# Optimization experiments

Hardware: AMD Instinct MI355X
Metric: run time of the kernel (lower is better)

## Reference

```python
import jax, jax.numpy as jnp
import numpy as np

B, L, D = 64, 4096, 256

def setup_inputs() -> dict:
    key = jax.random.key(0)
    k1, k2 = jax.random.split(key)
    inp = jax.random.normal(k1, (B, L, D), dtype=jnp.float32)
    # lengths in [1, L] so no empty-sequence mean (matches original assumption)
    length = jax.random.randint(k2, (B,), 1, L + 1, dtype=jnp.int64)
    return {"input": inp, "length": length}

def reference(input, length):
    # One fused masked mean over the ragged sequence dim.
    # mask: [B, L] True for valid positions
    mask = (jnp.arange(input.shape[1])[None, :] < length[:, None])
    m = mask.astype(input.dtype)[:, :, None]            # [B, L, 1]
    summed = jnp.sum(input * m, axis=1)                  # [B, D]
    return summed / length.astype(input.dtype)[:, None] # [B, D]
```

## Files before the change

kernel.cpp:

```cpp
#include <hip/hip_runtime.h>

#define BB 64
#define LL 4096
#define DD 256
#define D4 (DD / 4)
#define WAVES 4
#define RWAVES 8

template <int PP>
__global__ __launch_bounds__(256) void avg_partial_kernel(
    const float* __restrict__ in,
    const int* __restrict__ len,
    float* __restrict__ ws)
{
    constexpr int RPC = LL / PP;
    const int w    = threadIdx.x >> 6;
    const int lane = threadIdx.x & 63;
    const int c    = blockIdx.x * WAVES + w;
    const int b    = c / PP;
    const int p    = c % PP;

    const int lb   = len[b];
    const int row0 = p * RPC;
    if (row0 >= lb) return;

    int n = lb - row0;
    if (n > RPC) n = RPC;

    const float4* __restrict__ base =
        (const float4*)(in + (size_t)b * LL * DD) + (size_t)row0 * D4 + lane;

    float4 acc = make_float4(0.f, 0.f, 0.f, 0.f);
    #pragma unroll 8
    for (int r = 0; r < n; ++r) {
        float4 v = base[(size_t)r * D4];
        acc.x += v.x; acc.y += v.y; acc.z += v.z; acc.w += v.w;
    }

    float4* __restrict__ wsb = (float4*)ws + ((size_t)b * PP + p) * D4;
    wsb[lane] = acc;
}

template <int PP>
__global__ __launch_bounds__(512) void avg_reduce_kernel(
    const float* __restrict__ ws,
    const int* __restrict__ len,
    float* __restrict__ out)
{
    constexpr int RPC = LL / PP;
    const int b    = blockIdx.x;
    const int w    = threadIdx.x >> 6;
    const int lane = threadIdx.x & 63;

    int lb = len[b];
    if (lb < 1) lb = 1;
    const int nchunks = (lb + RPC - 1) / RPC;

    float4 acc = make_float4(0.f, 0.f, 0.f, 0.f);
    const float4* __restrict__ wsb = (const float4*)ws + (size_t)b * PP * D4;

    #pragma unroll 4
    for (int p = w; p < nchunks; p += RWAVES) {
        float4 v = wsb[(size_t)p * D4 + lane];
        acc.x += v.x; acc.y += v.y; acc.z += v.z; acc.w += v.w;
    }

    __shared__ float4 sh[RWAVES - 1][64];
    if (w > 0) sh[w - 1][lane] = acc;
    __syncthreads();

    if (w == 0) {
        #pragma unroll
        for (int i = 0; i < RWAVES - 1; ++i) {
            float4 v = sh[i][lane];
            acc.x += v.x; acc.y += v.y; acc.z += v.z; acc.w += v.w;
        }
        const float inv = 1.0f / (float)lb;
        float4 o = make_float4(acc.x * inv, acc.y * inv, acc.z * inv, acc.w * inv);
        ((float4*)out)[(size_t)b * D4 + lane] = o;
    }
}

__global__ void avg_zero_out_kernel(float* __restrict__ out) {
    int i = blockIdx.x * blockDim.x + threadIdx.x;
    if (i < BB * DD) out[i] = 0.f;
}

__global__ __launch_bounds__(64) void avg_atomic_kernel(
    const float* __restrict__ in,
    const int* __restrict__ len,
    float* __restrict__ out)
{
    const int b    = blockIdx.x >> 6;
    const int p    = blockIdx.x & 63;
    const int lane = threadIdx.x;

    int lb = len[b];
    if (lb < 1) lb = 1;
    const int row0 = p * 64;
    int rend = row0 + 64;
    if (rend > lb) rend = (lb > row0) ? lb : row0;
    if (rend <= row0) return;

    float4 acc = make_float4(0.f, 0.f, 0.f, 0.f);
    const float4* __restrict__ base = (const float4*)(in + (size_t)b * LL * DD);
    for (int r = row0; r < rend; ++r) {
        float4 v = base[(size_t)r * D4 + lane];
        acc.x += v.x; acc.y += v.y; acc.z += v.z; acc.w += v.w;
    }
    const float inv = 1.0f / (float)lb;
    float* o = out + (size_t)b * DD + lane * 4;
    atomicAdd(o + 0, acc.x * inv);
    atomicAdd(o + 1, acc.y * inv);
    atomicAdd(o + 2, acc.z * inv);
    atomicAdd(o + 3, acc.w * inv);
}

extern "C" void kernel_launch(void* const* d_in, const int* in_sizes, int n_in,
                              void* d_out, int out_size, void* d_ws, size_t ws_size,
                              hipStream_t stream) {
    const float* in  = (const float*)d_in[0];
    const int*   len = (const int*)d_in[1];
    float*       out = (float*)d_out;

    const size_t need128 = (size_t)BB * 128 * DD * sizeof(float);
    const size_t need64  = (size_t)BB * 64  * DD * sizeof(float);

    if (d_ws != nullptr && ws_size >= need128) {
        float* ws = (float*)d_ws;
        avg_partial_kernel<128><<<(BB * 128) / WAVES, 256, 0, stream>>>(in, len, ws);
        avg_reduce_kernel<128><<<BB, 64 * RWAVES, 0, stream>>>(ws, len, out);
    } else if (d_ws != nullptr && ws_size >= need64) {
        float* ws = (float*)d_ws;
        avg_partial_kernel<64><<<(BB * 64) / WAVES, 256, 0, stream>>>(in, len, ws);
        avg_reduce_kernel<64><<<BB, 64 * RWAVES, 0, stream>>>(ws, len, out);
    } else {
        avg_zero_out_kernel<<<(BB * DD + 255) / 256, 256, 0, stream>>>(out);
        avg_atomic_kernel<<<BB * 64, 64, 0, stream>>>(in, len, out);
    }
}
```

Measured before the change: 30.46 us.

## Compact work list of valid row chunks via prefix scan over lengths

New measurement: 32.46 us. 1.07x slower.

```diff
diff --git a/kernel.cpp b/kernel.cpp
--- a/kernel.cpp
+++ b/kernel.cpp
@@ -4,26 +4,54 @@
 #define LL 4096
 #define DD 256
 #define D4 (DD / 4)
-#define WAVES 4
+#define RPC 32
+#define CPB 4
+#define GRID1 2048
 #define RWAVES 8
 
-template <int PP>
+__device__ __forceinline__ void scan_prefix(const int* __restrict__ len,
+                                            int* pref, int tid) {
+    if (tid < 64) {
+        int lb = len[tid];
+        if (lb < 1) lb = 1;
+        int s = (lb + RPC - 1) >> 5;
+        #pragma unroll
+        for (int d = 1; d < 64; d <<= 1) {
+            int t = __shfl_up(s, d, 64);
+            if (tid >= d) s += t;
+        }
+        pref[tid + 1] = s;
+        if (tid == 0) pref[0] = 0;
+    }
+    __syncthreads();
+}
+
 __global__ __launch_bounds__(256) void avg_partial_kernel(
     const float* __restrict__ in,
     const int* __restrict__ len,
     float* __restrict__ ws)
 {
-    constexpr int RPC = LL / PP;
-    const int w    = threadIdx.x >> 6;
-    const int lane = threadIdx.x & 63;
-    const int c    = blockIdx.x * WAVES + w;
-    const int b    = c / PP;
-    const int p    = c % PP;
+    __shared__ int pref[BB + 1];
+    const int tid = threadIdx.x;
+    scan_prefix(len, pref, tid);
 
-    const int lb   = len[b];
+    const int A    = pref[BB];
+    const int w    = tid >> 6;
+    const int lane = tid & 63;
+    const int g    = blockIdx.x * CPB + w;
+    if (g >= A) return;
+
+    int lo = 0, hi = BB;
+    while (hi - lo > 1) {
+        int mid = (lo + hi) >> 1;
+        if (pref[mid] <= g) lo = mid; else hi = mid;
+    }
+    const int b = lo;
+    const int p = g - pref[b];
+
+    int lb = len[b];
+    if (lb < 1) lb = 1;
     const int row0 = p * RPC;
-    if (row0 >= lb) return;
-
     int n = lb - row0;
     if (n > RPC) n = RPC;
 
@@ -37,31 +65,27 @@
         acc.x += v.x; acc.y += v.y; acc.z += v.z; acc.w += v.w;
     }
 
-    float4* __restrict__ wsb = (float4*)ws + ((size_t)b * PP + p) * D4;
-    wsb[lane] = acc;
+    ((float4*)ws)[(size_t)g * D4 + lane] = acc;
 }
 
-template <int PP>
 __global__ __launch_bounds__(512) void avg_reduce_kernel(
     const float* __restrict__ ws,
     const int* __restrict__ len,
     float* __restrict__ out)
 {
-    constexpr int RPC = LL / PP;
+    __shared__ int pref[BB + 1];
+    const int tid = threadIdx.x;
+    scan_prefix(len, pref, tid);
+
     const int b    = blockIdx.x;
-    const int w    = threadIdx.x >> 6;
-    const int lane = threadIdx.x & 63;
-
-    int lb = len[b];
-    if (lb < 1) lb = 1;
-    const int nchunks = (lb + RPC - 1) / RPC;
+    const int w    = tid >> 6;
+    const int lane = tid & 63;
+    const int g0   = pref[b];
+    const int g1   = pref[b + 1];
 
     float4 acc = make_float4(0.f, 0.f, 0.f, 0.f);
-    const float4* __restrict__ wsb = (const float4*)ws + (size_t)b * PP * D4;
-
-    #pragma unroll 4
-    for (int p = w; p < nchunks; p += RWAVES) {
-        float4 v = wsb[(size_t)p * D4 + lane];
+    for (int g = g0 + w; g < g1; g += RWAVES) {
+        float4 v = ((const float4*)ws)[(size_t)g * D4 + lane];
         acc.x += v.x; acc.y += v.y; acc.z += v.z; acc.w += v.w;
     }
 
@@ -75,6 +99,8 @@
             float4 v = sh[i][lane];
             acc.x += v.x; acc.y += v.y; acc.z += v.z; acc.w += v.w;
         }
+        int lb = len[b];
+        if (lb < 1) lb = 1;
         const float inv = 1.0f / (float)lb;
         float4 o = make_float4(acc.x * inv, acc.y * inv, acc.z * inv, acc.w * inv);
         ((float4*)out)[(size_t)b * D4 + lane] = o;
@@ -123,17 +149,12 @@
     const int*   len = (const int*)d_in[1];
     float*       out = (float*)d_out;
 
-    const size_t need128 = (size_t)BB * 128 * DD * sizeof(float);
-    const size_t need64  = (size_t)BB * 64  * DD * sizeof(float);
+    const size_t ws_needed = (size_t)(BB * (LL / RPC)) * DD * sizeof(float);
 
-    if (d_ws != nullptr && ws_size >= need128) {
+    if (d_ws != nullptr && ws_size >= ws_needed) {
         float* ws = (float*)d_ws;
-        avg_partial_kernel<128><<<(BB * 128) / WAVES, 256, 0, stream>>>(in, len, ws);
-        avg_reduce_kernel<128><<<BB, 64 * RWAVES, 0, stream>>>(ws, len, out);
-    } else if (d_ws != nullptr && ws_size >= need64) {
-        float* ws = (float*)d_ws;
-        avg_partial_kernel<64><<<(BB * 64) / WAVES, 256, 0, stream>>>(in, len, ws);
-        avg_reduce_kernel<64><<<BB, 64 * RWAVES, 0, stream>>>(ws, len, out);
+        avg_partial_kernel<<<GRID1, 64 * CPB, 0, stream>>>(in, len, ws);
+        avg_reduce_kernel<<<BB, 64 * RWAVES, 0, stream>>>(ws, len, out);
     } else {
         avg_zero_out_kernel<<<(BB * DD + 255) / 256, 256, 0, stream>>>(out);
         avg_atomic_kernel<<<BB * 64, 64, 0, stream>>>(in, len, out);
```
